# Kernel tuning notes

Hardware: AMD Instinct MI355X
Metric: run time of the kernel (lower is better)

The kernel has to match this reference:

```python
import jax, jax.numpy as jnp
import numpy as np

B, S, D, NH = 4, 2048, 1024, 16
HD = D // NH


def setup_inputs() -> dict:
    key = jax.random.key(0)
    ks = jax.random.split(key, 8)
    inp = {
        'value': jax.random.normal(ks[0], (B, S, D), jnp.float32),
        'key_t': jax.random.normal(ks[1], (B, S, D), jnp.float32),
        'query': jax.random.normal(ks[2], (B, S, D), jnp.float32),
        'mask': jnp.ones((B, 1, 1, S), jnp.int32),
        # nn.Linear weights (stored as [out, in]; y = x @ W.T). bias=False for q/k/v.
        'W_q': jax.random.normal(ks[3], (D, D), jnp.float32) * (D ** -0.5),
        'W_k': jax.random.normal(ks[4], (D, D), jnp.float32) * (D ** -0.5),
        'W_v': jax.random.normal(ks[5], (D, D), jnp.float32) * (D ** -0.5),
        'W_o': jax.random.normal(ks[6], (D, D), jnp.float32) * (D ** -0.5),
        'b_o': jax.random.normal(ks[7], (D,), jnp.float32) * 0.01,
    }
    return inp


def _split_head(x):
    b, s, d = x.shape
    return x.reshape(b, s, NH, d // NH).transpose(0, 2, 1, 3)  # [B,NH,S,HD]


def reference(value, key_t, query, mask, W_q, W_k, W_v, W_o, b_o):
    # Linear projections (y = x @ W.T), then split heads
    q = _split_head(query @ W_q.T)  # [B,NH,S,HD]
    k = _split_head(key_t @ W_k.T)
    v = _split_head(value @ W_v.T)

    q = q * (HD ** -0.5)
    att = jnp.einsum('bhqd,bhkd->bhqk', q, k)  # [B,NH,S,S]
    att = jnp.where(mask == 0, -jnp.inf, att)
    att = jax.nn.softmax(att, axis=-1)
    # dropout_ratio = 0.0 -> identity (eval mode)
    ctx = jnp.einsum('bhqk,bhkd->bhqd', att, v)  # [B,NH,S,HD]

    ctx = ctx.transpose(0, 2, 1, 3).reshape(B, S, D)  # concat heads
    out = ctx @ W_o.T + b_o
    out = jax.nn.gelu(out, approximate=False)  # nn.GELU default = exact erf
    return out
```

## Files before the change

kernel.cpp:

```cpp
#include <hip/hip_runtime.h>
#include <hip/hip_bf16.h>

typedef __bf16 bf16;
typedef __bf16 bf16x8 __attribute__((ext_vector_type(8)));
typedef __bf16 bf16x4 __attribute__((ext_vector_type(4)));
typedef float f32x4 __attribute__((ext_vector_type(4)));
typedef float f32x16 __attribute__((ext_vector_type(16)));
typedef unsigned int uint;

#define NB 4
#define NS 2048
#define ND 1024
#define NHH 16
#define NHD 64

__device__ __forceinline__ void gload_lds16(const void* g, void* l) {
  __builtin_amdgcn_global_load_lds((const __attribute__((address_space(1))) void*)g,
                                   (__attribute__((address_space(3))) void*)l, 16, 0, 0);
}

__device__ __forceinline__ f32x4 mfma16(bf16x8 a, bf16x8 b, f32x4 c) {
  return __builtin_amdgcn_mfma_f32_16x16x32_bf16(a, b, c, 0, 0, 0);
}
__device__ __forceinline__ f32x16 mfma32(bf16x8 a, bf16x8 b, f32x16 c) {
  return __builtin_amdgcn_mfma_f32_32x32x16_bf16(a, b, c, 0, 0, 0);
}
__device__ __forceinline__ uint cvtpk(float lo, float hi) {
  uint r;
  asm("v_cvt_pk_bf16_f32 %0, %1, %2" : "=v"(r) : "v"(lo), "v"(hi));
  return r;
}
__device__ __forceinline__ void swap32u(uint& a, uint& b) {
  asm("v_permlane32_swap_b32 %0, %1" : "+v"(a), "+v"(b));
}
__device__ __forceinline__ float expv(float x) {
  float r;
  asm("v_exp_f32 %0, %1" : "=v"(r) : "v"(x));
  return r;
}
#define BARRIER()                          \
  do {                                     \
    asm volatile("" ::: "memory");         \
    __builtin_amdgcn_s_barrier();          \
    asm volatile("" ::: "memory");         \
  } while (0)

__global__ __launch_bounds__(256) void prep(
    const float4* __restrict__ w0, const float4* __restrict__ w1,
    const float4* __restrict__ w2, const float4* __restrict__ w3,
    bf16x4* __restrict__ wout, float scale0, int n4each,
    const int* __restrict__ m, float* __restrict__ mb,
    uint* __restrict__ cleanw, int nmask) {
  const int bid = blockIdx.x;
  if (bid < 4096) {
    int i = bid * 256 + threadIdx.x;
    int w = i / n4each;
    int j = i - w * n4each;
    const float4* src = (w == 0) ? w0 : (w == 1) ? w1 : (w == 2) ? w2 : w3;
    float sc = (w == 0) ? scale0 : 1.0f;
    float4 v = src[j];
    bf16x4 o;
    o[0] = (bf16)(v.x * sc);
    o[1] = (bf16)(v.y * sc);
    o[2] = (bf16)(v.z * sc);
    o[3] = (bf16)(v.w * sc);
    wout[i] = o;
  } else if (bid < 4128) {
    int i = (bid - 4096) * 256 + threadIdx.x;
    if (i < nmask) mb[i] = m[i] ? 0.0f : -3e38f;
  } else {
    int i = threadIdx.x;
    if (i < 128) {
      const int* p = m + i * 64;
      int all1 = 1;
#pragma unroll
      for (int j = 0; j < 64; j += 4) {
        int4 v = *(const int4*)(p + j);
        all1 &= (v.x && v.y && v.z && v.w) ? 1 : 0;
      }
      unsigned long long bal = __ballot(all1);
      int wv = i >> 6, lane = i & 63;
      if (lane == 0) {
        cleanw[2 * wv] = (uint)bal;
        cleanw[2 * wv + 1] = (uint)(bal >> 32);
      }
    }
  }
}

__global__ __launch_bounds__(256) void proj_gemm(
    const float* __restrict__ Aq, const float* __restrict__ Ak,
    const float* __restrict__ Av, const bf16* __restrict__ Wb,
    bf16* __restrict__ Qb, bf16* __restrict__ Kb, bf16* __restrict__ Vtb) {
  __shared__ bf16 As[2][128 * 32];
  __shared__ bf16 Bs[2][128 * 32];
  const int tid = threadIdx.x;
  const int lane = tid & 63, wv = tid >> 6;
  const int wr = wv >> 1, wc = wv & 1;
  const int g = lane >> 4, r = lane & 15;
  const int bid = blockIdx.x;
  const int wg = (bid & 7) * 192 + (bid >> 3);
  const int z = wg / 512;
  const int t = wg - z * 512;
  const int colBase = (t & 7) * 128;
  const int rowBase = (t >> 3) * 128;

  const float* A = (z == 0) ? Aq : (z == 1) ? Ak : Av;
  const bf16* Bw = Wb + (long)z * ND * ND;

  const float* ap[4];
#pragma unroll
  for (int j = 0; j < 4; j++) {
    int idx = j * 256 + tid;
    ap[j] = A + (long)(rowBase + (idx >> 3)) * ND + (idx & 7) * 4;
  }
  const int sRow = wv * 16 + (lane >> 2);
  const int sK = (lane & 3) * 8;
  const bf16* bSrc0 = Bw + (long)(colBase + sRow) * ND + sK;
  const bf16* bSrc1 = bSrc0 + 64L * ND;

#define LOADA(k0)                                              \
  do {                                                         \
    ar[0] = *(const float4*)(ap[0] + (k0));                    \
    ar[1] = *(const float4*)(ap[1] + (k0));                    \
    ar[2] = *(const float4*)(ap[2] + (k0));                    \
    ar[3] = *(const float4*)(ap[3] + (k0));                    \
  } while (0)
#define GLOADB(bi, k0)                                         \
  do {                                                         \
    gload_lds16(bSrc0 + (k0), &Bs[bi][0] + wv * 512);          \
    gload_lds16(bSrc1 + (k0), &Bs[bi][0] + 2048 + wv * 512);   \
  } while (0)
#define WRITEA(bi)                                             \
  do {                                                         \
    _Pragma("unroll") for (int j = 0; j < 4; j++) {            \
      int idx = j * 256 + tid;                                 \
      bf16x4 pk;                                               \
      pk[0] = (bf16)ar[j].x;                                   \
      pk[1] = (bf16)ar[j].y;                                   \
      pk[2] = (bf16)ar[j].z;                                   \
      pk[3] = (bf16)ar[j].w;                                   \
      *(bf16x4*)(&As[bi][0] + (idx >> 3) * 32 + (idx & 7) * 4) = pk; \
    }                                                          \
  } while (0)

  f32x4 acc[4][4] = {};
  float4 ar[4];

  LOADA(0);
  GLOADB(0, 0);
  asm volatile("s_waitcnt vmcnt(0)" ::: "memory");
  WRITEA(0);
  __syncthreads();

  int buf = 0;
  for (int k0 = 0; k0 < ND; k0 += 32) {
    const int more = (k0 + 32 < ND);
    if (more) {
      LOADA(k0 + 32);
      GLOADB(buf ^ 1, k0 + 32);
    }
    bf16x8 af[4], bfr[4];
#pragma unroll
    for (int m = 0; m < 4; m++)
      af[m] = *(const bf16x8*)(&As[buf][0] + (wr * 64 + m * 16 + r) * 32 + g * 8);
#pragma unroll
    for (int n = 0; n < 4; n++)
      bfr[n] = *(const bf16x8*)(&Bs[buf][0] + (wc * 64 + n * 16 + r) * 32 + g * 8);
    __builtin_amdgcn_s_setprio(1);
#pragma unroll
    for (int m = 0; m < 4; m++)
#pragma unroll
      for (int n = 0; n < 4; n++)
        acc[m][n] = mfma16(af[m], bfr[n], acc[m][n]);
    __builtin_amdgcn_s_setprio(0);
    if (more) {
      asm volatile("s_waitcnt vmcnt(0)" ::: "memory");
      WRITEA(buf ^ 1);
    }
    __syncthreads();
    buf ^= 1;
  }
#undef LOADA
#undef GLOADB
#undef WRITEA

  if (z <= 1) {
    bf16* C = z ? Kb : Qb;
#pragma unroll
    for (int m = 0; m < 4; m++)
#pragma unroll
      for (int n = 0; n < 4; n++)
#pragma unroll
        for (int q = 0; q < 4; q++) {
          int row = rowBase + wr * 64 + m * 16 + 4 * g + q;
          int col = colBase + wc * 64 + n * 16 + r;
          C[(long)row * ND + col] = (bf16)acc[m][n][q];
        }
  } else {
    const int b = rowBase >> 11;
    const int sbase = (rowBase & 2047) + wr * 64;
#pragma unroll
    for (int m = 0; m < 4; m++) {
#pragma unroll
      for (int n = 0; n < 4; n++) {
        int col = colBase + wc * 64 + n * 16 + r;
        int h = col >> 6, d = col & 63;
        bf16x4 pk;
#pragma unroll
        for (int q = 0; q < 4; q++) pk[q] = (bf16)acc[m][n][q];
        *(bf16x4*)(Vtb + ((long)(b * NHH + h) * NHD + d) * NS + sbase + m * 16 + 4 * g) = pk;
      }
    }
  }
}

__global__ __launch_bounds__(256) void gemm_out(
    const bf16* __restrict__ A, const bf16* __restrict__ Bw,
    float* __restrict__ Cf, const float* __restrict__ bias, int M, int N, int K) {
  __shared__ bf16 As[2][128 * 32];
  __shared__ bf16 Bs[2][64 * 32];
  bf16* As0 = &As[0][0];
  bf16* Bs0 = &Bs[0][0];
  const int tid = threadIdx.x;
  const int lane = tid & 63, wv = tid >> 6;
  const int wr = wv >> 1, wc = wv & 1;
  const int g = lane >> 4, r = lane & 15;
  const int nx = N >> 6;
  const int chunk = gridDim.x >> 3;
  const int bid = blockIdx.x;
  const int wg = (bid & 7) * chunk + (bid >> 3);
  const int colBase = (wg % nx) * 64;
  const int rowBase = (wg / nx) * 128;

  const int sR = lane >> 2;
  const int sC = (lane & 3) * 8;
  const bf16* aj0 = A + (long)(rowBase + wv * 32 + sR) * K + sC;
  const bf16* aj1 = A + (long)(rowBase + wv * 32 + 16 + sR) * K + sC;
  const bf16* bj = Bw + (long)(colBase + wv * 16 + sR) * K + sC;

#define GSTAGE(bi, kk)                                          \
  do {                                                          \
    gload_lds16(aj0 + (kk), As0 + (bi) * 4096 + wv * 1024);     \
    gload_lds16(aj1 + (kk), As0 + (bi) * 4096 + wv * 1024 + 512); \
    gload_lds16(bj + (kk), Bs0 + (bi) * 2048 + wv * 512);       \
  } while (0)

  f32x4 acc[4][2] = {};

  GSTAGE(0, 0);
  int cur = 0;
  for (int k0 = 0; k0 < K; k0 += 32) {
    asm volatile("s_waitcnt lgkmcnt(0)" ::: "memory");
    BARRIER();
    if (k0 + 32 < K) {
      GSTAGE(cur ^ 1, k0 + 32);
      asm volatile("s_waitcnt vmcnt(3)" ::: "memory");
    } else {
      asm volatile("s_waitcnt vmcnt(0)" ::: "memory");
    }
    BARRIER();
    __builtin_amdgcn_sched_barrier(0);
    const bf16* Ac = As0 + cur * 4096;
    const bf16* Bc = Bs0 + cur * 2048;
    bf16x8 af[4], bfr[2];
#pragma unroll
    for (int m = 0; m < 4; m++)
      af[m] = *(const bf16x8*)(Ac + (wr * 64 + m * 16 + r) * 32 + g * 8);
#pragma unroll
    for (int n = 0; n < 2; n++)
      bfr[n] = *(const bf16x8*)(Bc + (wc * 32 + n * 16 + r) * 32 + g * 8);
    __builtin_amdgcn_s_setprio(1);
#pragma unroll
    for (int m = 0; m < 4; m++)
#pragma unroll
      for (int n = 0; n < 2; n++)
        acc[m][n] = mfma16(af[m], bfr[n], acc[m][n]);
    __builtin_amdgcn_s_setprio(0);
    cur ^= 1;
  }
#undef GSTAGE

#pragma unroll
  for (int m = 0; m < 4; m++)
#pragma unroll
    for (int n = 0; n < 2; n++)
#pragma unroll
      for (int q = 0; q < 4; q++) {
        int row = rowBase + wr * 64 + m * 16 + 4 * g + q;
        int col = colBase + wc * 32 + n * 16 + r;
        float v = acc[m][n][q] + bias[col];
        v = 0.5f * v * (1.0f + erff(v * 0.70710678118654752f));
        Cf[(long)row * N + col] = v;
      }
}

__global__ __launch_bounds__(512) void attn_fwd4(
    const bf16* __restrict__ Q, const bf16* __restrict__ K,
    const bf16* __restrict__ Vt, const float* __restrict__ mbias,
    const uint* __restrict__ cleanw, bf16* __restrict__ ctx) {
  __shared__ bf16 Ks[3][64 * 64];
  __shared__ bf16 Vs[3][64 * 64];
  bf16* Ks0 = &Ks[0][0];
  bf16* Vs0 = &Vs[0][0];
  const int tid = threadIdx.x;
  const int lane = tid & 63, wv = tid >> 6;
  const int ql = lane & 31, hi = lane >> 5;
  const int g = blockIdx.x;
  const int gx = (g & 63) >> 3;
  const int bh = ((g >> 6) << 3) | (g & 7);
  const int b = bh >> 4, h = bh & 15;
  const int q0 = gx * 256 + wv * 32;

  const bf16* Qp = Q + ((long)(b * NS + q0 + ql)) * ND + h * NHD;
  const bf16* Kp = K + ((long)b * NS) * ND + h * NHD;
  const bf16* Vp = Vt + (long)bh * NHD * NS;
  const float* mbp = mbias + b * NS;
  const uint cw = cleanw[b];

  bf16x8 qf[4];
#pragma unroll
  for (int cd = 0; cd < 4; cd++)
    qf[cd] = *(const bf16x8*)(Qp + cd * 16 + hi * 8);

  f32x16 o[2] = {};
  float lrun = 0.f;

  const int Lrow = wv * 8 + (lane >> 3);
  const int scb = ((lane & 7) * 16) ^ ((Lrow & 7) << 4);
  const bf16* kS = Kp + (long)Lrow * ND + (scb >> 1);
  const bf16* vS = Vp + (long)Lrow * NS + (scb >> 1);

#define ASTAGE(bi, sv)                                        \
  do {                                                        \
    gload_lds16(kS + (long)(sv) * ND, Ks0 + (bi) * 4096 + wv * 512); \
    gload_lds16(vS + (sv), Vs0 + (bi) * 4096 + wv * 512);     \
  } while (0)

  const int swz = (ql & 7) << 4;

  ASTAGE(0, 0);
  int cur = 0, nxt = 1;

  for (int s0 = 0; s0 < NS; s0 += 64) {
    if (s0 + 64 < NS) {
      ASTAGE(nxt, s0 + 64);
      asm volatile("s_waitcnt vmcnt(2)" ::: "memory");
    } else {
      asm volatile("s_waitcnt vmcnt(0)" ::: "memory");
    }
    BARRIER();
    __builtin_amdgcn_sched_barrier(0);
    const char* KsB = (const char*)(Ks0 + cur * 4096);
    const char* VsB = (const char*)(Vs0 + cur * 4096);

    f32x16 st0 = {}, st1 = {};
    __builtin_amdgcn_s_setprio(1);
#pragma unroll
    for (int cd = 0; cd < 4; cd++) {
      bf16x8 kf0 = *(const bf16x8*)(KsB + ql * 128 + ((cd * 32 + hi * 16) ^ swz));
      st0 = mfma32(kf0, qf[cd], st0);
      bf16x8 kf1 = *(const bf16x8*)(KsB + (32 + ql) * 128 + ((cd * 32 + hi * 16) ^ swz));
      st1 = mfma32(kf1, qf[cd], st1);
    }
    __builtin_amdgcn_s_setprio(0);

    if (!((cw >> (s0 >> 6)) & 1)) {
#pragma unroll
      for (int t = 0; t < 4; t++) {
        float4 m0 = *(const float4*)(mbp + s0 + t * 8 + hi * 4);
        st0[4 * t + 0] += m0.x;
        st0[4 * t + 1] += m0.y;
        st0[4 * t + 2] += m0.z;
        st0[4 * t + 3] += m0.w;
        float4 m1 = *(const float4*)(mbp + s0 + 32 + t * 8 + hi * 4);
        st1[4 * t + 0] += m1.x;
        st1[4 * t + 1] += m1.y;
        st1[4 * t + 2] += m1.z;
        st1[4 * t + 3] += m1.w;
      }
    }

#pragma unroll
    for (int i = 0; i < 16; i++) {
      st0[i] = expv(st0[i]);
      st1[i] = expv(st1[i]);
    }
    float u[16];
#pragma unroll
    for (int i = 0; i < 16; i++) u[i] = st0[i] + st1[i];
#pragma unroll
    for (int off = 8; off; off >>= 1)
#pragma unroll
      for (int i = 0; i < off; i++) u[i] += u[i + off];
    lrun += u[0];

    union {
      uint u[16];
      bf16x8 f[4];
    } pw;
    {
      uint c0 = cvtpk(st0[0], st0[1]), c1 = cvtpk(st0[4], st0[5]);
      swap32u(c0, c1);
      uint d0 = cvtpk(st0[2], st0[3]), d1 = cvtpk(st0[6], st0[7]);
      swap32u(d0, d1);
      pw.u[0] = c0; pw.u[1] = d0; pw.u[2] = c1; pw.u[3] = d1;
      uint e0 = cvtpk(st0[8], st0[9]), e1 = cvtpk(st0[12], st0[13]);
      swap32u(e0, e1);
      uint f0 = cvtpk(st0[10], st0[11]), f1 = cvtpk(st0[14], st0[15]);
      swap32u(f0, f1);
      pw.u[4] = e0; pw.u[5] = f0; pw.u[6] = e1; pw.u[7] = f1;
    }
    {
      uint c0 = cvtpk(st1[0], st1[1]), c1 = cvtpk(st1[4], st1[5]);
      swap32u(c0, c1);
      uint d0 = cvtpk(st1[2], st1[3]), d1 = cvtpk(st1[6], st1[7]);
      swap32u(d0, d1);
      pw.u[8] = c0; pw.u[9] = d0; pw.u[10] = c1; pw.u[11] = d1;
      uint e0 = cvtpk(st1[8], st1[9]), e1 = cvtpk(st1[12], st1[13]);
      swap32u(e0, e1);
      uint f0 = cvtpk(st1[10], st1[11]), f1 = cvtpk(st1[14], st1[15]);
      swap32u(f0, f1);
      pw.u[12] = e0; pw.u[13] = f0; pw.u[14] = e1; pw.u[15] = f1;
    }

    __builtin_amdgcn_s_setprio(1);
#pragma unroll
    for (int dt = 0; dt < 2; dt++) {
#pragma unroll
      for (int ck = 0; ck < 4; ck++) {
        bf16x8 vf = *(const bf16x8*)(VsB + (dt * 32 + ql) * 128 +
                                     ((ck * 32 + hi * 16) ^ swz));
        o[dt] = mfma32(vf, pw.f[ck], o[dt]);
      }
    }
    __builtin_amdgcn_s_setprio(0);
    cur = nxt;
    nxt = (nxt == 2) ? 0 : nxt + 1;
  }
#undef ASTAGE

  lrun += __shfl_xor(lrun, 32);
  const float invL = 1.0f / lrun;
  bf16* op = ctx + ((long)(b * NS + q0 + ql)) * ND + h * NHD;
#pragma unroll
  for (int dt = 0; dt < 2; dt++) {
#pragma unroll
    for (int t = 0; t < 4; t++) {
      bf16x4 pk;
#pragma unroll
      for (int i = 0; i < 4; i++) pk[i] = (bf16)(o[dt][t * 4 + i] * invL);
      *(bf16x4*)(op + dt * 32 + t * 8 + hi * 4) = pk;
    }
  }
}

extern "C" void kernel_launch(void* const* d_in, const int* in_sizes, int n_in,
                              void* d_out, int out_size, void* d_ws, size_t ws_size,
                              hipStream_t stream) {
  const float* value = (const float*)d_in[0];
  const float* key_t = (const float*)d_in[1];
  const float* query = (const float*)d_in[2];
  const int* mask = (const int*)d_in[3];
  const float* W_q = (const float*)d_in[4];
  const float* W_k = (const float*)d_in[5];
  const float* W_v = (const float*)d_in[6];
  const float* W_o = (const float*)d_in[7];
  const float* b_o = (const float*)d_in[8];
  float* out = (float*)d_out;

  char* ws = (char*)d_ws;
  bf16* wb = (bf16*)(ws + 0);
  bf16* Qb = (bf16*)(ws + (8UL << 20));
  bf16* Kb = (bf16*)(ws + (24UL << 20));
  bf16* Vtb = (bf16*)(ws + (40UL << 20));
  bf16* ctx = (bf16*)(ws + (56UL << 20));
  float* mbias = (float*)(ws + (72UL << 20));
  uint* cleanwd = (uint*)(ws + (72UL << 20) + 32768);

  const int nW4 = (ND * ND) / 4;
  const float hscale = 0.125f * 1.44269504088896f;

  prep<<<4129, 256, 0, stream>>>((const float4*)W_q, (const float4*)W_k,
                                 (const float4*)W_v, (const float4*)W_o,
                                 (bf16x4*)wb, hscale, nW4,
                                 mask, mbias, cleanwd, NB * NS);
  bf16* wob = wb + 3L * ND * ND;

  proj_gemm<<<1536, 256, 0, stream>>>(query, key_t, value, wb, Qb, Kb, Vtb);

  attn_fwd4<<<512, 512, 0, stream>>>(Qb, Kb, Vtb, mbias, cleanwd, ctx);

  gemm_out<<<(ND / 64) * ((NB * NS) / 128), 256, 0, stream>>>(
      ctx, wob, out, b_o, NB * NS, ND, ND);
}
```

Measured before the change: 211.2 us.

## Deepen projection GEMM pipeline to prefetch two K-steps ahead

The QKV projection GEMM now issues global loads two K-tiles ahead, using a triple-buffered LDS B tile and two alternating register sets for the fp32 A tile. Partial vmcnt waits replace full drains, so one stage of loads can stay in flight while the current tile's MFMAs run. The goal is to hide global memory latency in the projection. In exchange it uses more LDS and more VGPRs, which may lower occupancy, and the hand-counted vmcnt values must match the real number of outstanding loads.

```diff
diff --git a/kernel.cpp b/kernel.cpp
--- a/kernel.cpp
+++ b/kernel.cpp
@@ -44,6 +44,7 @@
     __builtin_amdgcn_s_barrier();          \
     asm volatile("" ::: "memory");         \
   } while (0)
+#define LGKM_DRAIN() asm volatile("s_waitcnt lgkmcnt(0)" ::: "memory")
 
 __global__ __launch_bounds__(256) void prep(
     const float4* __restrict__ w0, const float4* __restrict__ w1,
@@ -93,7 +94,7 @@
     const float* __restrict__ Av, const bf16* __restrict__ Wb,
     bf16* __restrict__ Qb, bf16* __restrict__ Kb, bf16* __restrict__ Vtb) {
   __shared__ bf16 As[2][128 * 32];
-  __shared__ bf16 Bs[2][128 * 32];
+  __shared__ bf16 Bs[3][128 * 32];
   const int tid = threadIdx.x;
   const int lane = tid & 63, wv = tid >> 6;
   const int wr = wv >> 1, wc = wv & 1;
@@ -119,68 +120,85 @@
   const bf16* bSrc0 = Bw + (long)(colBase + sRow) * ND + sK;
   const bf16* bSrc1 = bSrc0 + 64L * ND;
 
-#define LOADA(k0)                                              \
+#define LOADA(R, k0)                                           \
   do {                                                         \
-    ar[0] = *(const float4*)(ap[0] + (k0));                    \
-    ar[1] = *(const float4*)(ap[1] + (k0));                    \
-    ar[2] = *(const float4*)(ap[2] + (k0));                    \
-    ar[3] = *(const float4*)(ap[3] + (k0));                    \
+    R[0] = *(const float4*)(ap[0] + (k0));                     \
+    R[1] = *(const float4*)(ap[1] + (k0));                     \
+    R[2] = *(const float4*)(ap[2] + (k0));                     \
+    R[3] = *(const float4*)(ap[3] + (k0));                     \
   } while (0)
 #define GLOADB(bi, k0)                                         \
   do {                                                         \
     gload_lds16(bSrc0 + (k0), &Bs[bi][0] + wv * 512);          \
     gload_lds16(bSrc1 + (k0), &Bs[bi][0] + 2048 + wv * 512);   \
   } while (0)
-#define WRITEA(bi)                                             \
+#define WRITEA(bi, R)                                          \
   do {                                                         \
     _Pragma("unroll") for (int j = 0; j < 4; j++) {            \
       int idx = j * 256 + tid;                                 \
       bf16x4 pk;                                               \
-      pk[0] = (bf16)ar[j].x;                                   \
-      pk[1] = (bf16)ar[j].y;                                   \
-      pk[2] = (bf16)ar[j].z;                                   \
-      pk[3] = (bf16)ar[j].w;                                   \
+      pk[0] = (bf16)R[j].x;                                    \
+      pk[1] = (bf16)R[j].y;                                    \
+      pk[2] = (bf16)R[j].z;                                    \
+      pk[3] = (bf16)R[j].w;                                    \
       *(bf16x4*)(&As[bi][0] + (idx >> 3) * 32 + (idx & 7) * 4) = pk; \
     }                                                          \
   } while (0)
 
   f32x4 acc[4][4] = {};
-  float4 ar[4];
-
-  LOADA(0);
+  float4 arA[4], arB[4];
+
+  LOADA(arA, 0);
   GLOADB(0, 0);
-  asm volatile("s_waitcnt vmcnt(0)" ::: "memory");
-  WRITEA(0);
-  __syncthreads();
-
-  int buf = 0;
-  for (int k0 = 0; k0 < ND; k0 += 32) {
-    const int more = (k0 + 32 < ND);
-    if (more) {
-      LOADA(k0 + 32);
-      GLOADB(buf ^ 1, k0 + 32);
-    }
-    bf16x8 af[4], bfr[4];
-#pragma unroll
-    for (int m = 0; m < 4; m++)
-      af[m] = *(const bf16x8*)(&As[buf][0] + (wr * 64 + m * 16 + r) * 32 + g * 8);
-#pragma unroll
-    for (int n = 0; n < 4; n++)
-      bfr[n] = *(const bf16x8*)(&Bs[buf][0] + (wc * 64 + n * 16 + r) * 32 + g * 8);
-    __builtin_amdgcn_s_setprio(1);
-#pragma unroll
-    for (int m = 0; m < 4; m++)
-#pragma unroll
-      for (int n = 0; n < 4; n++)
-        acc[m][n] = mfma16(af[m], bfr[n], acc[m][n]);
-    __builtin_amdgcn_s_setprio(0);
-    if (more) {
-      asm volatile("s_waitcnt vmcnt(0)" ::: "memory");
-      WRITEA(buf ^ 1);
-    }
-    __syncthreads();
-    buf ^= 1;
-  }
+  LOADA(arB, 32);
+  GLOADB(1, 32);
+  asm volatile("s_waitcnt vmcnt(6)" ::: "memory");
+  WRITEA(0, arA);
+  LGKM_DRAIN();
+  BARRIER();
+
+#define STEP(k0, PAR, BCUR, BN2, RLD, RWR)                                \
+  do {                                                                    \
+    const int more2 = ((k0) + 64 < ND);                                   \
+    const int more1 = ((k0) + 32 < ND);                                   \
+    if (more2) {                                                          \
+      LOADA(RLD, (k0) + 64);                                              \
+      GLOADB(BN2, (k0) + 64);                                             \
+    }                                                                     \
+    bf16x8 af[4], bfr[4];                                                 \
+    _Pragma("unroll") for (int m = 0; m < 4; m++)                         \
+        af[m] = *(const bf16x8*)(&As[PAR][0] +                            \
+                                 (wr * 64 + m * 16 + r) * 32 + g * 8);    \
+    _Pragma("unroll") for (int n = 0; n < 4; n++)                         \
+        bfr[n] = *(const bf16x8*)(&Bs[BCUR][0] +                          \
+                                  (wc * 64 + n * 16 + r) * 32 + g * 8);   \
+    __builtin_amdgcn_s_setprio(1);                                        \
+    _Pragma("unroll") for (int m = 0; m < 4; m++)                         \
+        _Pragma("unroll") for (int n = 0; n < 4; n++)                     \
+            acc[m][n] = mfma16(af[m], bfr[n], acc[m][n]);                 \
+    __builtin_amdgcn_s_setprio(0);                                        \
+    if (more1) {                                                          \
+      if (more2)                                                          \
+        asm volatile("s_waitcnt vmcnt(6)" ::: "memory");                  \
+      else                                                                \
+        asm volatile("s_waitcnt vmcnt(0)" ::: "memory");                  \
+      WRITEA(PAR ^ 1, RWR);                                               \
+    }                                                                     \
+    LGKM_DRAIN();                                                         \
+    BARRIER();                                                            \
+    __builtin_amdgcn_sched_barrier(0);                                    \
+  } while (0)
+
+  int bc = 0;
+  for (int k0 = 0; k0 < ND; k0 += 64) {
+    const int b0 = bc;
+    const int b1 = (bc + 1 == 3) ? 0 : bc + 1;
+    const int b2 = (bc + 2 >= 3) ? bc - 1 : bc + 2;
+    STEP(k0, 0, b0, b2, arA, arB);
+    STEP(k0 + 32, 1, b1, b0, arB, arA);
+    bc = b2;
+  }
+#undef STEP
 #undef LOADA
 #undef GLOADB
 #undef WRITEA
@@ -251,7 +269,7 @@
   GSTAGE(0, 0);
   int cur = 0;
   for (int k0 = 0; k0 < K; k0 += 32) {
-    asm volatile("s_waitcnt lgkmcnt(0)" ::: "memory");
+    LGKM_DRAIN();
     BARRIER();
     if (k0 + 32 < K) {
       GSTAGE(cur ^ 1, k0 + 32);
```

Measured after the change: 202.6 us. 1.04x faster.

## Load projection A operand directly into registers, skip LDS staging, swizzle B tile

Applied to the files above, without the earlier changes.

The projection GEMM stops staging the fp32 activation tile through LDS. Each wave now loads its own 32 rows straight from global memory into registers, converts them to bf16 in place and uses them as MFMA A fragments, so each wave covers 32x128 instead of 64x64. The B (weight) tile still goes through LDS via global_load_lds, now with an XOR swizzle on the slot to cut bank conflicts, and each B fragment read feeds two MFMAs. This removes the LDS writes and reads for A and halves shared memory, at the cost of a full vmcnt drain every k-step and four times more B fragment reads per wave.

```diff
diff --git a/kernel.cpp b/kernel.cpp
--- a/kernel.cpp
+++ b/kernel.cpp
@@ -44,6 +44,8 @@
     __builtin_amdgcn_s_barrier();          \
     asm volatile("" ::: "memory");         \
   } while (0)
+#define LGKM_DRAIN() asm volatile("s_waitcnt lgkmcnt(0)" ::: "memory")
+#define VM_DRAIN() asm volatile("s_waitcnt vmcnt(0)" ::: "memory")
 
 __global__ __launch_bounds__(256) void prep(
     const float4* __restrict__ w0, const float4* __restrict__ w1,
@@ -92,124 +94,102 @@
     const float* __restrict__ Aq, const float* __restrict__ Ak,
     const float* __restrict__ Av, const bf16* __restrict__ Wb,
     bf16* __restrict__ Qb, bf16* __restrict__ Kb, bf16* __restrict__ Vtb) {
-  __shared__ bf16 As[2][128 * 32];
-  __shared__ bf16 Bs[2][128 * 32];
+  __shared__ bf16 Bs[2][4096];
   const int tid = threadIdx.x;
   const int lane = tid & 63, wv = tid >> 6;
-  const int wr = wv >> 1, wc = wv & 1;
-  const int g = lane >> 4, r = lane & 15;
+  const int r = lane & 15, g = lane >> 4;
   const int bid = blockIdx.x;
   const int wg = (bid & 7) * 192 + (bid >> 3);
-  const int z = wg / 512;
-  const int t = wg - z * 512;
-  const int colBase = (t & 7) * 128;
-  const int rowBase = (t >> 3) * 128;
+  const int z = wg >> 9;
+  const int t5 = wg & 511;
+  const int rowTile = t5 >> 3;
+  const int colBase = (t5 & 7) * 128;
 
   const float* A = (z == 0) ? Aq : (z == 1) ? Ak : Av;
   const bf16* Bw = Wb + (long)z * ND * ND;
 
-  const float* ap[4];
-#pragma unroll
-  for (int j = 0; j < 4; j++) {
-    int idx = j * 256 + tid;
-    ap[j] = A + (long)(rowBase + (idx >> 3)) * ND + (idx & 7) * 4;
-  }
-  const int sRow = wv * 16 + (lane >> 2);
-  const int sK = (lane & 3) * 8;
-  const bf16* bSrc0 = Bw + (long)(colBase + sRow) * ND + sK;
-  const bf16* bSrc1 = bSrc0 + 64L * ND;
-
-#define LOADA(k0)                                              \
-  do {                                                         \
-    ar[0] = *(const float4*)(ap[0] + (k0));                    \
-    ar[1] = *(const float4*)(ap[1] + (k0));                    \
-    ar[2] = *(const float4*)(ap[2] + (k0));                    \
-    ar[3] = *(const float4*)(ap[3] + (k0));                    \
-  } while (0)
-#define GLOADB(bi, k0)                                         \
-  do {                                                         \
-    gload_lds16(bSrc0 + (k0), &Bs[bi][0] + wv * 512);          \
-    gload_lds16(bSrc1 + (k0), &Bs[bi][0] + 2048 + wv * 512);   \
-  } while (0)
-#define WRITEA(bi)                                             \
-  do {                                                         \
-    _Pragma("unroll") for (int j = 0; j < 4; j++) {            \
-      int idx = j * 256 + tid;                                 \
-      bf16x4 pk;                                               \
-      pk[0] = (bf16)ar[j].x;                                   \
-      pk[1] = (bf16)ar[j].y;                                   \
-      pk[2] = (bf16)ar[j].z;                                   \
-      pk[3] = (bf16)ar[j].w;                                   \
-      *(bf16x4*)(&As[bi][0] + (idx >> 3) * 32 + (idx & 7) * 4) = pk; \
-    }                                                          \
-  } while (0)
-
-  f32x4 acc[4][4] = {};
-  float4 ar[4];
-
-  LOADA(0);
-  GLOADB(0, 0);
-  asm volatile("s_waitcnt vmcnt(0)" ::: "memory");
-  WRITEA(0);
-  __syncthreads();
-
-  int buf = 0;
-  for (int k0 = 0; k0 < ND; k0 += 32) {
-    const int more = (k0 + 32 < ND);
-    if (more) {
-      LOADA(k0 + 32);
-      GLOADB(buf ^ 1, k0 + 32);
-    }
-    bf16x8 af[4], bfr[4];
-#pragma unroll
-    for (int m = 0; m < 4; m++)
-      af[m] = *(const bf16x8*)(&As[buf][0] + (wr * 64 + m * 16 + r) * 32 + g * 8);
-#pragma unroll
-    for (int n = 0; n < 4; n++)
-      bfr[n] = *(const bf16x8*)(&Bs[buf][0] + (wc * 64 + n * 16 + r) * 32 + g * 8);
-    __builtin_amdgcn_s_setprio(1);
-#pragma unroll
-    for (int m = 0; m < 4; m++)
-#pragma unroll
-      for (int n = 0; n < 4; n++)
-        acc[m][n] = mfma16(af[m], bfr[n], acc[m][n]);
-    __builtin_amdgcn_s_setprio(0);
-    if (more) {
-      asm volatile("s_waitcnt vmcnt(0)" ::: "memory");
-      WRITEA(buf ^ 1);
-    }
-    __syncthreads();
-    buf ^= 1;
-  }
-#undef LOADA
-#undef GLOADB
-#undef WRITEA
+  const float* aBase0 = A + (long)(rowTile * 128 + wv * 32 + r) * ND + 8 * g;
+  const float* aBase1 = aBase0 + 16L * ND;
+
+  const int brow = wv * 16 + (lane >> 2);
+  const int bslot = (lane & 3) ^ ((lane >> 3) & 3);
+  const bf16* bsrc0 = Bw + (long)(colBase + brow) * ND + 8 * bslot;
+  const bf16* bsrc1 = Bw + (long)(colBase + brow + 64) * ND + 8 * bslot;
+  bf16* BsE = &Bs[0][0];
+
+  const int rdoff = r * 64 + ((g ^ ((r >> 1) & 3)) << 4);
+
+  f32x4 acc[2][8] = {};
+
+  float4 a0 = *(const float4*)(aBase0);
+  float4 a1 = *(const float4*)(aBase0 + 4);
+  float4 a2 = *(const float4*)(aBase1);
+  float4 a3 = *(const float4*)(aBase1 + 4);
+  gload_lds16(bsrc0, BsE + wv * 512);
+  gload_lds16(bsrc1, BsE + 2048 + wv * 512);
+
+  for (int t = 0; t < 32; t++) {
+    LGKM_DRAIN();
+    VM_DRAIN();
+    BARRIER();
+
+    bf16x8 af0, af1;
+    af0[0] = (bf16)a0.x; af0[1] = (bf16)a0.y;
+    af0[2] = (bf16)a0.z; af0[3] = (bf16)a0.w;
+    af0[4] = (bf16)a1.x; af0[5] = (bf16)a1.y;
+    af0[6] = (bf16)a1.z; af0[7] = (bf16)a1.w;
+    af1[0] = (bf16)a2.x; af1[1] = (bf16)a2.y;
+    af1[2] = (bf16)a2.z; af1[3] = (bf16)a2.w;
+    af1[4] = (bf16)a3.x; af1[5] = (bf16)a3.y;
+    af1[6] = (bf16)a3.z; af1[7] = (bf16)a3.w;
+
+    if (t + 1 < 32) {
+      const int k1 = (t + 1) * 32;
+      const int nb = (t + 1) & 1;
+      gload_lds16(bsrc0 + k1, BsE + nb * 4096 + wv * 512);
+      gload_lds16(bsrc1 + k1, BsE + nb * 4096 + 2048 + wv * 512);
+      a0 = *(const float4*)(aBase0 + k1);
+      a1 = *(const float4*)(aBase0 + k1 + 4);
+      a2 = *(const float4*)(aBase1 + k1);
+      a3 = *(const float4*)(aBase1 + k1 + 4);
+    }
+
+    const char* Bp = (const char*)BsE + (t & 1) * 8192 + rdoff;
+#pragma unroll
+    for (int n = 0; n < 8; n++) {
+      bf16x8 bfr = *(const bf16x8*)(Bp + n * 1024);
+      acc[0][n] = mfma16(af0, bfr, acc[0][n]);
+      acc[1][n] = mfma16(af1, bfr, acc[1][n]);
+    }
+  }
 
   if (z <= 1) {
     bf16* C = z ? Kb : Qb;
 #pragma unroll
-    for (int m = 0; m < 4; m++)
-#pragma unroll
-      for (int n = 0; n < 4; n++)
+    for (int m = 0; m < 2; m++)
+#pragma unroll
+      for (int n = 0; n < 8; n++)
 #pragma unroll
         for (int q = 0; q < 4; q++) {
-          int row = rowBase + wr * 64 + m * 16 + 4 * g + q;
-          int col = colBase + wc * 64 + n * 16 + r;
+          int row = rowTile * 128 + wv * 32 + m * 16 + 4 * g + q;
+          int col = colBase + n * 16 + r;
           C[(long)row * ND + col] = (bf16)acc[m][n][q];
         }
   } else {
-    const int b = rowBase >> 11;
-    const int sbase = (rowBase & 2047) + wr * 64;
-#pragma unroll
-    for (int m = 0; m < 4; m++) {
-#pragma unroll
-      for (int n = 0; n < 4; n++) {
-        int col = colBase + wc * 64 + n * 16 + r;
+    const int rw = rowTile * 128;
+    const int b = rw >> 11;
+    const int sbase = (rw & 2047) + wv * 32;
+#pragma unroll
+    for (int m = 0; m < 2; m++) {
+#pragma unroll
+      for (int n = 0; n < 8; n++) {
+        int col = colBase + n * 16 + r;
         int h = col >> 6, d = col & 63;
+        int s = sbase + m * 16 + 4 * g;
         bf16x4 pk;
 #pragma unroll
         for (int q = 0; q < 4; q++) pk[q] = (bf16)acc[m][n][q];
-        *(bf16x4*)(Vtb + ((long)(b * NHH + h) * NHD + d) * NS + sbase + m * 16 + 4 * g) = pk;
+        *(bf16x4*)(Vtb + ((long)(b * NHH + h) * NHD + d) * NS + s) = pk;
       }
     }
   }
@@ -251,13 +231,13 @@
   GSTAGE(0, 0);
   int cur = 0;
   for (int k0 = 0; k0 < K; k0 += 32) {
-    asm volatile("s_waitcnt lgkmcnt(0)" ::: "memory");
+    LGKM_DRAIN();
     BARRIER();
     if (k0 + 32 < K) {
       GSTAGE(cur ^ 1, k0 + 32);
       asm volatile("s_waitcnt vmcnt(3)" ::: "memory");
     } else {
-      asm volatile("s_waitcnt vmcnt(0)" ::: "memory");
+      VM_DRAIN();
     }
     BARRIER();
     __builtin_amdgcn_sched_barrier(0);
@@ -347,7 +327,7 @@
       ASTAGE(nxt, s0 + 64);
       asm volatile("s_waitcnt vmcnt(2)" ::: "memory");
     } else {
-      asm volatile("s_waitcnt vmcnt(0)" ::: "memory");
+      VM_DRAIN();
     }
     BARRIER();
     __builtin_amdgcn_sched_barrier(0);
```

Result: slower. 230.7 us (+9.2%).
